# Performance work log

Hardware: AMD Instinct MI355X
Metric: run time of the kernel (lower is better)

Reference implementation:

```python
import jax, jax.numpy as jnp
import numpy as np

DEPTH, HEADS, K, EPS = 4, 8, 3, 1e-5
DIM, CIN, COUT = 128, 64, 64


def conv1x1(x, w, b=None):
    y = jnp.einsum('oi,bihw->bohw', w, x)
    return y if b is None else y + b[None, :, None, None]


def dilated_conv3x3(x, w, b, d):
    y = jax.lax.conv_general_dilated(
        x, w, window_strides=(1, 1), padding=[(d, d), (d, d)],
        rhs_dilation=(d, d), dimension_numbers=('NCHW', 'OIHW', 'NCHW'))
    return y + b[None, :, None, None]


def batchnorm_train(x, g, b):
    # BatchNorm2d in training mode: biased batch stats over (B,H,W)
    mu = jnp.mean(x, axis=(0, 2, 3), keepdims=True)
    var = jnp.var(x, axis=(0, 2, 3), keepdims=True)
    return (x - mu) * jax.lax.rsqrt(var + EPS) * g[None, :, None, None] + b[None, :, None, None]


def unfold3(x):
    # nn.Unfold(k=3, pad=1): (B,C,H,W) -> (B,C,k*k,H,W), patch index row-major (dy,dx)
    B, C, H, W = x.shape
    p = K // 2
    xp = jnp.pad(x, ((0, 0), (0, 0), (p, p), (p, p)))
    return jnp.stack([xp[:, :, dy:dy + H, dx:dx + W]
                      for dy in range(K) for dx in range(K)], axis=2)


def local_self_attention(x, qkv_w, fc_w, fc_b):
    B, C, H, W = x.shape
    c = C // HEADS
    scale = c ** -0.5
    qkv = conv1x1(x, qkv_w)                      # (B,3C,H,W)
    q, k, v = jnp.split(qkv, 3, axis=1)
    shape6 = lambda t: unfold3(t).reshape(B, HEADS, c, K * K, H, W)
    q, k, v = shape6(q) * scale, shape6(k), shape6(v)
    # NOTE: original einsum labels dim2 (channels/head) as n/m and dim3 (k^2) as the
    # contracted axis, i.e. channel-attention contracted over the 9 patch positions.
    dots = jnp.einsum('bhnkij,bhmkij->bhnmij', q, k)   # (B,h,c,c,H,W)
    attn = jax.nn.softmax(dots, axis=3)
    out = jnp.einsum('bhnmij,bhmkij->bhnkij', attn, v)  # (B,h,c,k^2,H,W)
    out = out.reshape(B, C, K * K, H, W).sum(axis=2)
    return conv1x1(out, fc_w, fc_b) + x


def setup_inputs() -> dict:
    key = jax.random.key(0)
    ks = jax.random.split(key, 12)
    s = 0.05
    return {
        'x': jax.random.normal(ks[0], (2, CIN, 96, 96), jnp.float32),
        'w_in': jax.random.normal(ks[1], (DIM, CIN), jnp.float32) * s,
        'b_in': jnp.zeros((DIM,), jnp.float32),
        'conv_w': jax.random.normal(ks[2], (DEPTH, DIM, DIM, 3, 3), jnp.float32) * s,
        'conv_b': jnp.zeros((DEPTH, DIM), jnp.float32),
        'bn_g': jnp.ones((DEPTH, DIM), jnp.float32),
        'bn_b': jnp.zeros((DEPTH, DIM), jnp.float32),
        'qkv_w': jax.random.normal(ks[3], (DEPTH, 3 * DIM, DIM), jnp.float32) * s,
        'fc_w': jax.random.normal(ks[4], (DEPTH, DIM, DIM), jnp.float32) * s,
        'fc_b': jnp.zeros((DEPTH, DIM), jnp.float32),
        'w_out': jax.random.normal(ks[5], (COUT, DIM), jnp.float32) * s,
        'b_out': jnp.zeros((COUT,), jnp.float32),
    }


def reference(x, w_in, b_in, conv_w, conv_b, bn_g, bn_b, qkv_w, fc_w, fc_b, w_out, b_out):
    h = conv1x1(x, w_in, b_in)
    for i in range(DEPTH):
        d = 2 ** i
        h = jax.nn.relu(batchnorm_train(dilated_conv3x3(h, conv_w[i], conv_b[i], d), bn_g[i], bn_b[i]))
        h = local_self_attention(h, qkv_w[i], fc_w[i], fc_b[i])
    return conv1x1(h, w_out, b_out)
```

## Files before the change

### kernel.cpp

```cpp
#include <hip/hip_runtime.h>
#include <math.h>

typedef __attribute__((ext_vector_type(8))) short bf16x8;
typedef __attribute__((ext_vector_type(4))) float f32x4;
typedef __attribute__((ext_vector_type(4))) unsigned short us4;
typedef __attribute__((ext_vector_type(8))) unsigned short us8;

constexpr int BB = 2;
constexpr int CC = 128;
constexpr int HH = 96, WW = 96;
constexpr int PP = HH * WW;
constexpr int NN = BB * PP;
constexpr int CONV_BLKS = NN / 48;

__device__ __forceinline__ float bf2f(unsigned short u) {
    return __uint_as_float(((unsigned)u) << 16);
}
__device__ __forceinline__ unsigned short f2bf(float f) {
    unsigned u = __float_as_uint(f);
    unsigned r = u + 0x7fff + ((u >> 16) & 1);
    return (unsigned short)(r >> 16);
}

__global__ __launch_bounds__(256)
void k_wconv(const float* __restrict__ conv_w, const float* __restrict__ qkv_w,
             const float* __restrict__ fc_w, const float* __restrict__ w_in,
             const float* __restrict__ w_out,
             unsigned short* __restrict__ wcv, unsigned short* __restrict__ wqkv,
             unsigned short* __restrict__ wfc, unsigned short* __restrict__ wi,
             unsigned short* __restrict__ wo)
{
    int gid = blockIdx.x * 256 + threadIdx.x;
    if (gid < 589824) {
        int L = gid / 147456, r = gid % 147456;
        int o = r / 1152, k = r % 1152;
        int t = k / 128, c = k % 128;
        float v = conv_w[(((size_t)(L * 128 + o) * 128 + c) * 9) + t];
        wcv[gid] = f2bf(v);
    } else if (gid < 786432) {
        int g = gid - 589824;
        int o = (g % 49152) / 128;
        float v = qkv_w[g] * (o < 128 ? 0.25f : 1.0f);
        wqkv[g] = f2bf(v);
    } else if (gid < 851968) {
        int g = gid - 786432;
        wfc[g] = f2bf(fc_w[g]);
    } else if (gid < 860160) {
        int g = gid - 851968;
        wi[g] = f2bf(w_in[g]);
    } else if (gid < 868352) {
        int g = gid - 860160;
        wo[g] = f2bf(w_out[g]);
    }
}

__global__ __launch_bounds__(256)
void k_xconv(const float* __restrict__ x, unsigned short* __restrict__ xT)
{
    int n = blockIdx.x * 256 + threadIdx.x;
    int b = n / PP, p = n - b * PP;
    unsigned short* dst = xT + (size_t)n * 64;
    #pragma unroll
    for (int cg = 0; cg < 16; ++cg) {
        us4 st;
        #pragma unroll
        for (int r = 0; r < 4; ++r)
            st[r] = f2bf(x[((size_t)(b * 64 + cg * 4 + r)) * PP + p]);
        *reinterpret_cast<us4*>(dst + cg * 4) = st;
    }
}

template<int DIL>
__global__ __launch_bounds__(192)
void k_conv(const unsigned short* __restrict__ W,
            const unsigned short* __restrict__ act,
            float* __restrict__ y,
            float* __restrict__ parts,
            const unsigned short* __restrict__ zp)
{
    int tid = threadIdx.x;
    int lane = tid & 63, wz = tid >> 6;
    int l15 = lane & 15, kg = lane >> 4;

    int n_base = blockIdx.x * 48;
    int o_base = blockIdx.y * 32;

    const unsigned short* wbase[2];
    #pragma unroll
    for (int fm = 0; fm < 2; ++fm)
        wbase[fm] = W + (size_t)(o_base + fm * 16 + l15) * 1152 + kg * 8;

    const unsigned short* bbase[3];
    int iF[3], jF[3];
    #pragma unroll
    for (int fn = 0; fn < 3; ++fn) {
        int n = n_base + fn * 16 + l15;
        bbase[fn] = act + (size_t)n * 128 + kg * 8;
        int pix = n % PP;
        iF[fn] = pix / WW;
        jF[fn] = pix % WW;
    }

    f32x4 acc[2][3];
    #pragma unroll
    for (int fm = 0; fm < 2; ++fm)
        #pragma unroll
        for (int fn = 0; fn < 3; ++fn)
            acc[fm][fn] = (f32x4){0.f, 0.f, 0.f, 0.f};

    const unsigned short* zpk = zp + kg * 8;
    int t0 = wz * 3;
    #pragma unroll
    for (int tt = 0; tt < 3; ++tt) {
        int t = t0 + tt;
        int oy = (t / 3 - 1) * DIL, ox = (t % 3 - 1) * DIL;
        int disp = (oy * WW + ox) * 128;
        const unsigned short* baddr[3];
        #pragma unroll
        for (int fn = 0; fn < 3; ++fn) {
            bool v = ((unsigned)(iF[fn] + oy) < (unsigned)HH) &&
                     ((unsigned)(jF[fn] + ox) < (unsigned)WW);
            baddr[fn] = v ? (bbase[fn] + disp) : zpk;
        }
        #pragma unroll
        for (int c0 = 0; c0 < 128; c0 += 32) {
            bf16x8 a[2], b[3];
            #pragma unroll
            for (int fm = 0; fm < 2; ++fm)
                a[fm] = *reinterpret_cast<const bf16x8*>(wbase[fm] + t * 128 + c0);
            #pragma unroll
            for (int fn = 0; fn < 3; ++fn)
                b[fn] = *reinterpret_cast<const bf16x8*>(baddr[fn] + c0);
            #pragma unroll
            for (int fm = 0; fm < 2; ++fm)
                #pragma unroll
                for (int fn = 0; fn < 3; ++fn)
                    acc[fm][fn] = __builtin_amdgcn_mfma_f32_16x16x32_bf16(
                        a[fm], b[fn], acc[fm][fn], 0, 0, 0);
        }
    }

    __shared__ float red[2][24][64];
    if (wz) {
        #pragma unroll
        for (int fm = 0; fm < 2; ++fm)
            #pragma unroll
            for (int fn = 0; fn < 3; ++fn)
                #pragma unroll
                for (int r = 0; r < 4; ++r)
                    red[wz - 1][fm * 12 + fn * 4 + r][lane] = acc[fm][fn][r];
    }
    __syncthreads();
    if (wz == 0) {
        #pragma unroll
        for (int fm = 0; fm < 2; ++fm)
            #pragma unroll
            for (int fn = 0; fn < 3; ++fn)
                #pragma unroll
                for (int r = 0; r < 4; ++r)
                    acc[fm][fn][r] += red[0][fm * 12 + fn * 4 + r][lane] +
                                      red[1][fm * 12 + fn * 4 + r][lane];

        #pragma unroll
        for (int fm = 0; fm < 2; ++fm) {
            int o0 = o_base + fm * 16 + kg * 4;
            #pragma unroll
            for (int fn = 0; fn < 3; ++fn) {
                int n = n_base + fn * 16 + l15;
                *reinterpret_cast<f32x4*>(y + (size_t)n * 128 + o0) = acc[fm][fn];
            }
        }

        #pragma unroll
        for (int fm = 0; fm < 2; ++fm) {
            #pragma unroll
            for (int r = 0; r < 4; ++r) {
                float s = 0.f, s2 = 0.f;
                #pragma unroll
                for (int fn = 0; fn < 3; ++fn) {
                    float v = acc[fm][fn][r];
                    s += v; s2 += v * v;
                }
                #pragma unroll
                for (int m = 1; m <= 8; m <<= 1) {
                    s  += __shfl_xor(s,  m, 64);
                    s2 += __shfl_xor(s2, m, 64);
                }
                if (l15 == 0) {
                    int c = o_base + fm * 16 + kg * 4 + r;
                    parts[(size_t)blockIdx.x * 256 + c]       = s;
                    parts[(size_t)blockIdx.x * 256 + 128 + c] = s2;
                }
            }
        }
    }
}

template<int WM, int WN, int F, int MODE>
__global__ __launch_bounds__(WM * WN * 64)
void k_gemm(const unsigned short* __restrict__ W,
            const unsigned short* __restrict__ act,
            const float* __restrict__ bias,
            const unsigned short* __restrict__ resid,
            void* __restrict__ outp,
            int Kw, int Cin, int Cout)
{
    int tid = threadIdx.x;
    int lane = tid & 63, wv = tid >> 6;
    int wm = wv % WM, wn = wv / WM;
    int l15 = lane & 15, kg = lane >> 4;

    int n_base = blockIdx.x * (WN * 16 * F) + wn * 16 * F;
    int o_base = blockIdx.y * (WM * 64) + wm * 64;

    const unsigned short* wbase[4];
    #pragma unroll
    for (int fm = 0; fm < 4; ++fm) {
        int o = o_base + fm * 16 + l15;
        wbase[fm] = W + (size_t)o * Kw + kg * 8;
    }

    const unsigned short* bbase[F];
    #pragma unroll
    for (int fn = 0; fn < F; ++fn) {
        int n = n_base + fn * 16 + l15;
        bbase[fn] = act + (size_t)n * Cin + kg * 8;
    }

    f32x4 acc[4][F];
    #pragma unroll
    for (int fm = 0; fm < 4; ++fm)
        #pragma unroll
        for (int fn = 0; fn < F; ++fn)
            acc[fm][fn] = (f32x4){0.f, 0.f, 0.f, 0.f};

    #pragma unroll
    for (int k0 = 0; k0 < 128; k0 += 32) {
        if (k0 >= Cin) break;
        bf16x8 a[4], b[F];
        #pragma unroll
        for (int fm = 0; fm < 4; ++fm)
            a[fm] = *reinterpret_cast<const bf16x8*>(wbase[fm] + k0);
        #pragma unroll
        for (int fn = 0; fn < F; ++fn)
            b[fn] = *reinterpret_cast<const bf16x8*>(bbase[fn] + k0);
        #pragma unroll
        for (int fm = 0; fm < 4; ++fm)
            #pragma unroll
            for (int fn = 0; fn < F; ++fn)
                acc[fm][fn] = __builtin_amdgcn_mfma_f32_16x16x32_bf16(
                    a[fm], b[fn], acc[fm][fn], 0, 0, 0);
    }

    #pragma unroll
    for (int fm = 0; fm < 4; ++fm) {
        #pragma unroll
        for (int fn = 0; fn < F; ++fn) {
            f32x4 v = acc[fm][fn];
            int n = n_base + fn * 16 + l15;
            int o0 = o_base + fm * 16 + kg * 4;
            if constexpr (MODE == 0 || MODE == 2) {
                if (bias) {
                    #pragma unroll
                    for (int r = 0; r < 4; ++r) v[r] += bias[o0 + r];
                }
                if constexpr (MODE == 2) {
                    us4 rv = *reinterpret_cast<const us4*>(resid + (size_t)n * Cout + o0);
                    #pragma unroll
                    for (int r = 0; r < 4; ++r) v[r] += bf2f(rv[r]);
                }
                us4 st;
                #pragma unroll
                for (int r = 0; r < 4; ++r) st[r] = f2bf(v[r]);
                *reinterpret_cast<us4*>((unsigned short*)outp + (size_t)n * Cout + o0) = st;
            } else {
                int b_ = n / PP, p = n - b_ * PP;
                float* op = (float*)outp;
                #pragma unroll
                for (int r = 0; r < 4; ++r)
                    op[((size_t)(b_ * Cout + o0 + r)) * PP + p] = v[r] + bias[o0 + r];
            }
        }
    }
}

__global__ __launch_bounds__(384)
void k_bnfin(const float* __restrict__ partials, const float* __restrict__ g,
             const float* __restrict__ b, float* __restrict__ scsh)
{
    int c = blockIdx.x;
    int t = threadIdx.x;
    float s  = partials[(size_t)t * 256 + c];
    float s2 = partials[(size_t)t * 256 + 128 + c];
    #pragma unroll
    for (int m = 32; m > 0; m >>= 1) {
        s  += __shfl_down(s,  m, 64);
        s2 += __shfl_down(s2, m, 64);
    }
    __shared__ float ls[6], ls2[6];
    int wid = t >> 6;
    if ((t & 63) == 0) { ls[wid] = s; ls2[wid] = s2; }
    __syncthreads();
    if (t == 0) {
        float S = 0.f, S2 = 0.f;
        #pragma unroll
        for (int w = 0; w < 6; ++w) { S += ls[w]; S2 += ls2[w]; }
        const float inv = 1.f / (float)NN;
        float mu = S * inv;
        float var = S2 * inv - mu * mu;
        float sc = g[c] * rsqrtf(var + 1e-5f);
        scsh[c] = sc;
        scsh[128 + c] = b[c] - mu * sc;
    }
}

__global__ __launch_bounds__(256)
void k_bnrelu(const float* __restrict__ y, const float* __restrict__ scsh,
              unsigned short* __restrict__ h)
{
    int gid = blockIdx.x * 256 + threadIdx.x;
    int c0 = (gid * 4) & 127;
    size_t idx = (size_t)gid * 4;
    f32x4 v = *reinterpret_cast<const f32x4*>(y + idx);
    us4 st;
    #pragma unroll
    for (int r = 0; r < 4; ++r) {
        float f = fmaxf(fmaf(v[r], scsh[c0 + r], scsh[128 + c0 + r]), 0.f);
        st[r] = f2bf(f);
    }
    *reinterpret_cast<us4*>(h + idx) = st;
}

__global__ __launch_bounds__(192)
void k_attn2(const unsigned short* __restrict__ qkv, unsigned short* __restrict__ att)
{
    __shared__ unsigned short tile[294 * 56];
    int tid = threadIdx.x;
    int br = blockIdx.x;
    int head = blockIdx.y;
    int b = br / HH, i = br - b * HH;

    #pragma unroll
    for (int it = 0; it < 10; ++it) {
        int idx = it * 192 + tid;
        if (idx < 1764) {
            int pp = idx / 6;
            int rem = idx - pp * 6;
            int s = rem >> 1, u8 = rem & 1;
            int rr = pp / 98, cc = pp - rr * 98;
            int ai = i + rr - 1, aj = cc - 1;
            us8 val = {0, 0, 0, 0, 0, 0, 0, 0};
            if (((unsigned)ai < (unsigned)HH) && ((unsigned)aj < (unsigned)WW)) {
                int n = b * PP + ai * WW + aj;
                val = *reinterpret_cast<const us8*>(
                    qkv + (size_t)n * 384 + s * 128 + head * 16 + u8 * 8);
            }
            *reinterpret_cast<us8*>(tile + pp * 56 + s * 16 + u8 * 8) = val;
        }
    }
    __syncthreads();

    #pragma unroll
    for (int u = 0; u < 2; ++u) {
        int unit = u * 192 + tid;
        int j  = unit >> 2;
        int ng = unit & 3;

        float dots[4][16];
        #pragma unroll
        for (int nn = 0; nn < 4; ++nn)
            #pragma unroll
            for (int m = 0; m < 16; ++m) dots[nn][m] = 0.f;

        #pragma unroll
        for (int rr = 0; rr < 3; ++rr) {
            #pragma unroll
            for (int dj = 0; dj < 3; ++dj) {
                const unsigned short* pb = tile + (rr * 98 + j + dj) * 56;
                us4 q4 = *reinterpret_cast<const us4*>(pb + ng * 4);
                us8 k0 = *reinterpret_cast<const us8*>(pb + 16);
                us8 k1 = *reinterpret_cast<const us8*>(pb + 24);
                float kf[16];
                #pragma unroll
                for (int e = 0; e < 8; ++e) {
                    kf[e] = bf2f(k0[e]);
                    kf[8 + e] = bf2f(k1[e]);
                }
                #pragma unroll
                for (int nn = 0; nn < 4; ++nn) {
                    float qf = bf2f(q4[nn]);
                    #pragma unroll
                    for (int m = 0; m < 16; ++m)
                        dots[nn][m] = fmaf(qf, kf[m], dots[nn][m]);
                }
            }
        }

        float vs[16];
        #pragma unroll
        for (int m = 0; m < 16; ++m) vs[m] = 0.f;
        #pragma unroll
        for (int rr = 0; rr < 3; ++rr) {
            #pragma unroll
            for (int dj = 0; dj < 3; ++dj) {
                const unsigned short* pb = tile + (rr * 98 + j + dj) * 56;
                us8 v0 = *reinterpret_cast<const us8*>(pb + 32);
                us8 v1 = *reinterpret_cast<const us8*>(pb + 40);
                #pragma unroll
                for (int e = 0; e < 8; ++e) {
                    vs[e] += bf2f(v0[e]);
                    vs[8 + e] += bf2f(v1[e]);
                }
            }
        }

        us4 st;
        #pragma unroll
        for (int nn = 0; nn < 4; ++nn) {
            float mx = dots[nn][0];
            #pragma unroll
            for (int m = 1; m < 16; ++m) mx = fmaxf(mx, dots[nn][m]);
            float den = 0.f, o = 0.f;
            #pragma unroll
            for (int m = 0; m < 16; ++m) {
                float e = __expf(dots[nn][m] - mx);
                den += e;
                o = fmaf(e, vs[m], o);
            }
            st[nn] = f2bf(o / den);
        }
        int n = b * PP + i * WW + j;
        *reinterpret_cast<us4*>(att + (size_t)n * CC + head * 16 + ng * 4) = st;
    }
}

extern "C" void kernel_launch(void* const* d_in, const int* in_sizes, int n_in,
                              void* d_out, int out_size, void* d_ws, size_t ws_size,
                              hipStream_t stream)
{
    const float* x      = (const float*)d_in[0];
    const float* w_in   = (const float*)d_in[1];
    const float* b_in   = (const float*)d_in[2];
    const float* conv_w = (const float*)d_in[3];
    const float* bn_g   = (const float*)d_in[5];
    const float* bn_b   = (const float*)d_in[6];
    const float* qkv_w  = (const float*)d_in[7];
    const float* fc_w   = (const float*)d_in[8];
    const float* fc_b   = (const float*)d_in[9];
    const float* w_out  = (const float*)d_in[10];
    const float* b_out  = (const float*)d_in[11];

    char* ws = (char*)d_ws;
    unsigned short* zp    = (unsigned short*)(ws);
    unsigned short* wcv   = (unsigned short*)(ws + 4096);
    unsigned short* wqkv  = (unsigned short*)(ws + 1183744);
    unsigned short* wfc   = (unsigned short*)(ws + 1576960);
    unsigned short* wi    = (unsigned short*)(ws + 1708032);
    unsigned short* wo    = (unsigned short*)(ws + 1724416);
    unsigned short* xT    = (unsigned short*)(ws + 1740800);
    unsigned short* bufA  = (unsigned short*)(ws + 4100096);
    float*          ybuf  = (float*)        (ws + 8818688);
    unsigned short* hbuf  = (unsigned short*)(ws + 18255872);
    unsigned short* qkvb  = (unsigned short*)(ws + 22974464);
    unsigned short* attb  = (unsigned short*)(ws + 37130240);
    float*          parts = (float*)        (ws + 41848832);
    float*          scsh  = (float*)        (ws + 42242048);

    hipMemsetAsync(zp, 0, 4096, stream);

    k_wconv<<<3392, 256, 0, stream>>>(conv_w, qkv_w, fc_w, w_in, w_out,
                                      wcv, wqkv, wfc, wi, wo);
    k_xconv<<<NN / 256, 256, 0, stream>>>(x, xT);

    k_gemm<1, 2, 3, 0><<<dim3(192, 2), 128, 0, stream>>>(
        wi, xT, b_in, nullptr, bufA, 64, 64, 128);

    for (int L = 0; L < 4; ++L) {
        const unsigned short* wc = wcv + (size_t)L * 147456;
        switch (L) {
            case 0: k_conv<1><<<dim3(CONV_BLKS, 4), 192, 0, stream>>>(wc, bufA, ybuf, parts, zp); break;
            case 1: k_conv<2><<<dim3(CONV_BLKS, 4), 192, 0, stream>>>(wc, bufA, ybuf, parts, zp); break;
            case 2: k_conv<4><<<dim3(CONV_BLKS, 4), 192, 0, stream>>>(wc, bufA, ybuf, parts, zp); break;
            case 3: k_conv<8><<<dim3(CONV_BLKS, 4), 192, 0, stream>>>(wc, bufA, ybuf, parts, zp); break;
        }
        k_bnfin<<<128, 384, 0, stream>>>(parts, bn_g + L * 128, bn_b + L * 128, scsh);
        k_bnrelu<<<2304, 256, 0, stream>>>(ybuf, scsh, hbuf);

        k_gemm<1, 2, 3, 0><<<dim3(192, 6), 128, 0, stream>>>(
            wqkv + (size_t)L * 49152, hbuf, nullptr, nullptr, qkvb, 128, 128, 384);

        k_attn2<<<dim3(BB * HH, 8), 192, 0, stream>>>(qkvb, attb);

        k_gemm<1, 2, 3, 2><<<dim3(192, 2), 128, 0, stream>>>(
            wfc + (size_t)L * 16384, attb, fc_b + L * 128, hbuf, bufA, 128, 128, 128);
    }

    k_gemm<1, 2, 3, 3><<<dim3(192, 1), 128, 0, stream>>>(
        wo, bufA, b_out, nullptr, (float*)d_out, 128, 128, 64);
}
```

Baseline: 481.8 us.

## Fuse BN+ReLU into qkv GEMM and residual, widen conv output tile to 64

Removes the standalone BN+ReLU kernel and its bf16 h buffer. The qkv GEMM now reads fp32 conv output and applies scale/shift/ReLU on load, and the fc GEMM recomputes the activation for its residual add. Separately, the dilated conv blocks now cover 64 output channels instead of 32, halving grid.y and reusing activation loads across more MFMAs. This trades one launch and a write/read pass for fp32 loads (twice the bytes) in the GEMM, and a larger register and LDS footprint in the conv.

```diff
diff --git a/kernel.cpp b/kernel.cpp
--- a/kernel.cpp
+++ b/kernel.cpp
@@ -83,11 +83,11 @@
     int l15 = lane & 15, kg = lane >> 4;
 
     int n_base = blockIdx.x * 48;
-    int o_base = blockIdx.y * 32;
-
-    const unsigned short* wbase[2];
-    #pragma unroll
-    for (int fm = 0; fm < 2; ++fm)
+    int o_base = blockIdx.y * 64;
+
+    const unsigned short* wbase[4];
+    #pragma unroll
+    for (int fm = 0; fm < 4; ++fm)
         wbase[fm] = W + (size_t)(o_base + fm * 16 + l15) * 1152 + kg * 8;
 
     const unsigned short* bbase[3];
@@ -101,9 +101,9 @@
         jF[fn] = pix % WW;
     }
 
-    f32x4 acc[2][3];
-    #pragma unroll
-    for (int fm = 0; fm < 2; ++fm)
+    f32x4 acc[4][3];
+    #pragma unroll
+    for (int fm = 0; fm < 4; ++fm)
         #pragma unroll
         for (int fn = 0; fn < 3; ++fn)
             acc[fm][fn] = (f32x4){0.f, 0.f, 0.f, 0.f};
@@ -124,15 +124,15 @@
         }
         #pragma unroll
         for (int c0 = 0; c0 < 128; c0 += 32) {
-            bf16x8 a[2], b[3];
-            #pragma unroll
-            for (int fm = 0; fm < 2; ++fm)
+            bf16x8 a[4], b[3];
+            #pragma unroll
+            for (int fm = 0; fm < 4; ++fm)
                 a[fm] = *reinterpret_cast<const bf16x8*>(wbase[fm] + t * 128 + c0);
             #pragma unroll
             for (int fn = 0; fn < 3; ++fn)
                 b[fn] = *reinterpret_cast<const bf16x8*>(baddr[fn] + c0);
             #pragma unroll
-            for (int fm = 0; fm < 2; ++fm)
+            for (int fm = 0; fm < 4; ++fm)
                 #pragma unroll
                 for (int fn = 0; fn < 3; ++fn)
                     acc[fm][fn] = __builtin_amdgcn_mfma_f32_16x16x32_bf16(
@@ -140,10 +140,10 @@
         }
     }
 
-    __shared__ float red[2][24][64];
+    __shared__ float red[2][48][64];
     if (wz) {
         #pragma unroll
-        for (int fm = 0; fm < 2; ++fm)
+        for (int fm = 0; fm < 4; ++fm)
             #pragma unroll
             for (int fn = 0; fn < 3; ++fn)
                 #pragma unroll
@@ -153,7 +153,7 @@
     __syncthreads();
     if (wz == 0) {
         #pragma unroll
-        for (int fm = 0; fm < 2; ++fm)
+        for (int fm = 0; fm < 4; ++fm)
             #pragma unroll
             for (int fn = 0; fn < 3; ++fn)
                 #pragma unroll
@@ -162,7 +162,7 @@
                                       red[1][fm * 12 + fn * 4 + r][lane];
 
         #pragma unroll
-        for (int fm = 0; fm < 2; ++fm) {
+        for (int fm = 0; fm < 4; ++fm) {
             int o0 = o_base + fm * 16 + kg * 4;
             #pragma unroll
             for (int fn = 0; fn < 3; ++fn) {
@@ -172,7 +172,7 @@
         }
 
         #pragma unroll
-        for (int fm = 0; fm < 2; ++fm) {
+        for (int fm = 0; fm < 4; ++fm) {
             #pragma unroll
             for (int r = 0; r < 4; ++r) {
                 float s = 0.f, s2 = 0.f;
@@ -196,12 +196,13 @@
     }
 }
 
-template<int WM, int WN, int F, int MODE>
+template<int WM, int WN, int F, int MODE, int BNIN>
 __global__ __launch_bounds__(WM * WN * 64)
 void k_gemm(const unsigned short* __restrict__ W,
             const unsigned short* __restrict__ act,
+            const float* __restrict__ y,
+            const float* __restrict__ scsh,
             const float* __restrict__ bias,
-            const unsigned short* __restrict__ resid,
             void* __restrict__ outp,
             int Kw, int Cin, int Cout)
 {
@@ -221,10 +222,14 @@
     }
 
     const unsigned short* bbase[F];
+    const float* ybase[F];
     #pragma unroll
     for (int fn = 0; fn < F; ++fn) {
         int n = n_base + fn * 16 + l15;
-        bbase[fn] = act + (size_t)n * Cin + kg * 8;
+        if constexpr (BNIN)
+            ybase[fn] = y + (size_t)n * 128 + kg * 8;
+        else
+            bbase[fn] = act + (size_t)n * Cin + kg * 8;
     }
 
     f32x4 acc[4][F];
@@ -241,9 +246,28 @@
         #pragma unroll
         for (int fm = 0; fm < 4; ++fm)
             a[fm] = *reinterpret_cast<const bf16x8*>(wbase[fm] + k0);
-        #pragma unroll
-        for (int fn = 0; fn < F; ++fn)
-            b[fn] = *reinterpret_cast<const bf16x8*>(bbase[fn] + k0);
+        if constexpr (BNIN) {
+            f32x4 sc0 = *reinterpret_cast<const f32x4*>(scsh + k0 + kg * 8);
+            f32x4 sc1 = *reinterpret_cast<const f32x4*>(scsh + k0 + kg * 8 + 4);
+            f32x4 sh0 = *reinterpret_cast<const f32x4*>(scsh + 128 + k0 + kg * 8);
+            f32x4 sh1 = *reinterpret_cast<const f32x4*>(scsh + 128 + k0 + kg * 8 + 4);
+            #pragma unroll
+            for (int fn = 0; fn < F; ++fn) {
+                f32x4 u0 = *reinterpret_cast<const f32x4*>(ybase[fn] + k0);
+                f32x4 u1 = *reinterpret_cast<const f32x4*>(ybase[fn] + k0 + 4);
+                bf16x8 bb;
+                #pragma unroll
+                for (int e = 0; e < 4; ++e) {
+                    bb[e]     = (short)f2bf(fmaxf(fmaf(u0[e], sc0[e], sh0[e]), 0.f));
+                    bb[4 + e] = (short)f2bf(fmaxf(fmaf(u1[e], sc1[e], sh1[e]), 0.f));
+                }
+                b[fn] = bb;
+            }
+        } else {
+            #pragma unroll
+            for (int fn = 0; fn < F; ++fn)
+                b[fn] = *reinterpret_cast<const bf16x8*>(bbase[fn] + k0);
+        }
         #pragma unroll
         for (int fm = 0; fm < 4; ++fm)
             #pragma unroll
@@ -265,9 +289,10 @@
                     for (int r = 0; r < 4; ++r) v[r] += bias[o0 + r];
                 }
                 if constexpr (MODE == 2) {
-                    us4 rv = *reinterpret_cast<const us4*>(resid + (size_t)n * Cout + o0);
+                    f32x4 yv = *reinterpret_cast<const f32x4*>(y + (size_t)n * 128 + o0);
                     #pragma unroll
-                    for (int r = 0; r < 4; ++r) v[r] += bf2f(rv[r]);
+                    for (int r = 0; r < 4; ++r)
+                        v[r] += fmaxf(fmaf(yv[r], scsh[o0 + r], scsh[128 + o0 + r]), 0.f);
                 }
                 us4 st;
                 #pragma unroll
@@ -312,23 +337,6 @@
         scsh[c] = sc;
         scsh[128 + c] = b[c] - mu * sc;
     }
-}
-
-__global__ __launch_bounds__(256)
-void k_bnrelu(const float* __restrict__ y, const float* __restrict__ scsh,
-              unsigned short* __restrict__ h)
-{
-    int gid = blockIdx.x * 256 + threadIdx.x;
-    int c0 = (gid * 4) & 127;
-    size_t idx = (size_t)gid * 4;
-    f32x4 v = *reinterpret_cast<const f32x4*>(y + idx);
-    us4 st;
-    #pragma unroll
-    for (int r = 0; r < 4; ++r) {
-        float f = fmaxf(fmaf(v[r], scsh[c0 + r], scsh[128 + c0 + r]), 0.f);
-        st[r] = f2bf(f);
-    }
-    *reinterpret_cast<us4*>(h + idx) = st;
 }
 
 __global__ __launch_bounds__(192)
@@ -460,7 +468,6 @@
     unsigned short* xT    = (unsigned short*)(ws + 1740800);
     unsigned short* bufA  = (unsigned short*)(ws + 4100096);
     float*          ybuf  = (float*)        (ws + 8818688);
-    unsigned short* hbuf  = (unsigned short*)(ws + 18255872);
     unsigned short* qkvb  = (unsigned short*)(ws + 22974464);
     unsigned short* attb  = (unsigned short*)(ws + 37130240);
     float*          parts = (float*)        (ws + 41848832);
@@ -472,29 +479,28 @@
                                       wcv, wqkv, wfc, wi, wo);
     k_xconv<<<NN / 256, 256, 0, stream>>>(x, xT);
 
-    k_gemm<1, 2, 3, 0><<<dim3(192, 2), 128, 0, stream>>>(
-        wi, xT, b_in, nullptr, bufA, 64, 64, 128);
+    k_gemm<1, 2, 3, 0, 0><<<dim3(192, 2), 128, 0, stream>>>(
+        wi, xT, nullptr, nullptr, b_in, bufA, 64, 64, 128);
 
     for (int L = 0; L < 4; ++L) {
         const unsigned short* wc = wcv + (size_t)L * 147456;
         switch (L) {
-            case 0: k_conv<1><<<dim3(CONV_BLKS, 4), 192, 0, stream>>>(wc, bufA, ybuf, parts, zp); break;
-            case 1: k_conv<2><<<dim3(CONV_BLKS, 4), 192, 0, stream>>>(wc, bufA, ybuf, parts, zp); break;
-            case 2: k_conv<4><<<dim3(CONV_BLKS, 4), 192, 0, stream>>>(wc, bufA, ybuf, parts, zp); break;
-            case 3: k_conv<8><<<dim3(CONV_BLKS, 4), 192, 0, stream>>>(wc, bufA, ybuf, parts, zp); break;
+            case 0: k_conv<1><<<dim3(CONV_BLKS, 2), 192, 0, stream>>>(wc, bufA, ybuf, parts, zp); break;
+            case 1: k_conv<2><<<dim3(CONV_BLKS, 2), 192, 0, stream>>>(wc, bufA, ybuf, parts, zp); break;
+            case 2: k_conv<4><<<dim3(CONV_BLKS, 2), 192, 0, stream>>>(wc, bufA, ybuf, parts, zp); break;
+            case 3: k_conv<8><<<dim3(CONV_BLKS, 2), 192, 0, stream>>>(wc, bufA, ybuf, parts, zp); break;
         }
         k_bnfin<<<128, 384, 0, stream>>>(parts, bn_g + L * 128, bn_b + L * 128, scsh);
-        k_bnrelu<<<2304, 256, 0, stream>>>(ybuf, scsh, hbuf);
-
-        k_gemm<1, 2, 3, 0><<<dim3(192, 6), 128, 0, stream>>>(
-            wqkv + (size_t)L * 49152, hbuf, nullptr, nullptr, qkvb, 128, 128, 384);
+
+        k_gemm<1, 2, 3, 0, 1><<<dim3(192, 6), 128, 0, stream>>>(
+            wqkv + (size_t)L * 49152, nullptr, ybuf, scsh, nullptr, qkvb, 128, 128, 384);
 
         k_attn2<<<dim3(BB * HH, 8), 192, 0, stream>>>(qkvb, attb);
 
-        k_gemm<1, 2, 3, 2><<<dim3(192, 2), 128, 0, stream>>>(
-            wfc + (size_t)L * 16384, attb, fc_b + L * 128, hbuf, bufA, 128, 128, 128);
-    }
-
-    k_gemm<1, 2, 3, 3><<<dim3(192, 1), 128, 0, stream>>>(
-        wo, bufA, b_out, nullptr, (float*)d_out, 128, 128, 64);
-}
+        k_gemm<1, 2, 3, 2, 0><<<dim3(192, 2), 128, 0, stream>>>(
+            wfc + (size_t)L * 16384, attb, ybuf, scsh, fc_b + L * 128, bufA, 128, 128, 128);
+    }
+
+    k_gemm<1, 2, 3, 3, 0><<<dim3(192, 1), 128, 0, stream>>>(
+        wo, bufA, nullptr, nullptr, b_out, (float*)d_out, 128, 128, 64);
+}
```

New measurement: 474.1 us. About the same (-1.6%).
